# Optimization experiments

Measured on AMD Instinct MI355X. Metric: run time of the kernel, lower is better.

## Reference

```python
import jax, jax.numpy as jnp
import numpy as np


def _conv(x, w, stride):
    # Conv2d(k=3, stride, padding=1, bias=False), NCHW/OIHW
    return jax.lax.conv_general_dilated(
        x, w, (stride, stride), ((1, 1), (1, 1)),
        dimension_numbers=('NCHW', 'OIHW', 'NCHW'))


def _bn_silu(x, g, b, m, v):
    # BatchNorm2d (inference) + SiLU, fused elementwise
    scale = (g * jax.lax.rsqrt(v + 1e-5))[None, :, None, None]
    y = (x - m[None, :, None, None]) * scale + b[None, :, None, None]
    return y * jax.nn.sigmoid(y)


def _ss2d(x, in_w, dt_w, dt_b, B_w, C_w, A_log, D, out_w):
    # Low-rank 2D selective scan over flattened spatial tokens.
    Bn, C, H, W = x.shape
    L = H * W
    xt = x.reshape(Bn, C, L).transpose(0, 2, 1)            # [B,L,C]
    u = jnp.einsum('blc,rc->blr', xt, in_w)                # low-rank input [B,L,R]
    dt = jax.nn.softplus(jnp.einsum('blc,rc->blr', xt, dt_w) + dt_b)
    Bt = jnp.einsum('blc,nc->bln', xt, B_w)                # [B,L,N]
    Ct = jnp.einsum('blc,nc->bln', xt, C_w)                # [B,L,N]
    A = -jnp.exp(A_log)                                    # [R,N], stable (negative)

    def step(h, inp):
        u_t, dt_t, b_t, c_t = inp                          # [B,R],[B,R],[B,N],[B,N]
        dA = jnp.exp(dt_t[..., None] * A)                  # [B,R,N]
        h = dA * h + (dt_t[..., None] * b_t[:, None, :]) * u_t[..., None]
        y = jnp.einsum('brn,bn->br', h, c_t)               # [B,R]
        return h, (h, y)

    R, N = A_log.shape
    h0 = jnp.zeros((Bn, R, N), x.dtype)
    xs = (u.transpose(1, 0, 2), dt.transpose(1, 0, 2),
          Bt.transpose(1, 0, 2), Ct.transpose(1, 0, 2))
    _, (hs, ys) = jax.lax.scan(step, h0, xs)               # hs:[L,B,R,N] ys:[L,B,R]
    y = ys.transpose(1, 0, 2) + D * u                      # skip term D*u
    out = jnp.einsum('blr,cr->blc', y, out_w)              # project back to C
    x_out = (xt + out).transpose(0, 2, 1).reshape(Bn, C, H, W)
    state_seq = hs.transpose(1, 0, 2, 3)                   # [B,L,R,N]
    return x_out, state_seq


def setup_inputs() -> dict:
    key = jax.random.key(0)
    ks = jax.random.split(key, 24)
    f = jax.random.normal
    B, Cin, H, W = 8, 32, 112, 112
    E, R, N, NB = 64, 32, 64, 3
    inp = {}
    inp['x'] = f(ks[0], (B, Cin, H, W), jnp.float32)
    # stem
    inp['stem_w'] = f(ks[1], (E, Cin, 3, 3)) * 0.05
    inp['stem_g'] = 1.0 + 0.1 * f(ks[2], (E,))
    inp['stem_b'] = 0.1 * f(ks[3], (E,))
    inp['stem_m'] = 0.1 * f(ks[4], (E,))
    inp['stem_v'] = 1.0 + 0.1 * jax.random.uniform(ks[5], (E,))
    # SS2D blocks (stacked over num_blocks)
    inp['blk_in_w'] = f(ks[6], (NB, R, E)) * 0.1
    inp['blk_dt_w'] = f(ks[7], (NB, R, E)) * 0.05
    inp['blk_dt_b'] = f(ks[8], (NB, R)) * 0.1 - 2.0
    inp['blk_B_w'] = f(ks[9], (NB, N, E)) * 0.1
    inp['blk_C_w'] = f(ks[10], (NB, N, E)) * 0.1
    inp['blk_A_log'] = jnp.log(1.0 + jax.random.uniform(ks[11], (NB, R, N)) * 4.0)
    inp['blk_D'] = f(ks[12], (NB, R)) * 0.1
    inp['blk_out_w'] = f(ks[13], (NB, E, R)) * 0.1
    # down p4
    C4, C5 = 2 * E, 4 * E
    inp['p4_w'] = f(ks[14], (C4, E, 3, 3)) * 0.05
    inp['p4_g'] = 1.0 + 0.1 * f(ks[15], (C4,))
    inp['p4_b'] = 0.1 * f(ks[16], (C4,))
    inp['p4_m'] = 0.1 * f(ks[17], (C4,))
    inp['p4_v'] = 1.0 + 0.1 * jax.random.uniform(ks[18], (C4,))
    # down p5
    inp['p5_w'] = f(ks[19], (C5, C4, 3, 3)) * 0.05
    inp['p5_g'] = 1.0 + 0.1 * f(ks[20], (C5,))
    inp['p5_b'] = 0.1 * f(ks[21], (C5,))
    inp['p5_m'] = 0.1 * f(ks[22], (C5,))
    inp['p5_v'] = 1.0 + 0.1 * jax.random.uniform(ks[23], (C5,))
    return inp


def reference(x, stem_w, stem_g, stem_b, stem_m, stem_v,
              blk_in_w, blk_dt_w, blk_dt_b, blk_B_w, blk_C_w,
              blk_A_log, blk_D, blk_out_w,
              p4_w, p4_g, p4_b, p4_m, p4_v,
              p5_w, p5_g, p5_b, p5_m, p5_v):
    x = _bn_silu(_conv(x, stem_w, 2), stem_g, stem_b, stem_m, stem_v)
    states = []
    for i in range(blk_in_w.shape[0]):
        x, s = _ss2d(x, blk_in_w[i], blk_dt_w[i], blk_dt_b[i],
                     blk_B_w[i], blk_C_w[i], blk_A_log[i], blk_D[i], blk_out_w[i])
        states.append(s)
    p3 = x
    p4 = _bn_silu(_conv(p3, p4_w, 2), p4_g, p4_b, p4_m, p4_v)
    p5 = _bn_silu(_conv(p4, p5_w, 2), p5_g, p5_b, p5_m, p5_v)
    return (p3, p4, p5, jnp.stack(states))
```

## Files before the change

### kernel.cpp

```cpp
#include <hip/hip_runtime.h>
#include <cstdint>
#include <cstddef>

#define RFL(x) __builtin_amdgcn_readfirstlane(x)

constexpr int E  = 64;
constexpr int Rr = 32;
constexpr int Nn = 64;
constexpr int Lt = 3136;
constexpr int NC = 28;
constexpr int CL = 112;
constexpr int PD = 192;

__global__ __launch_bounds__(256) void k_wtrans(const float* __restrict__ in_w,
    const float* __restrict__ dt_w, const float* __restrict__ B_w,
    const float* __restrict__ C_w, float* __restrict__ wT) {
  int idx = blockIdx.x * 256 + threadIdx.x;
  if (idx >= 3 * 64 * PD) return;
  int o = idx % PD; int c = (idx / PD) & 63; int i = idx / (PD * 64);
  float v;
  if (o < 32)       v = in_w[(i * 32 + o) * 64 + c];
  else if (o < 64)  v = dt_w[(i * 32 + (o - 32)) * 64 + c];
  else if (o < 128) v = B_w[(i * 64 + (o - 64)) * 64 + c];
  else              v = C_w[(i * 64 + (o - 128)) * 64 + c];
  wT[idx] = v;
}

__global__ __launch_bounds__(256) void k_cwt2(const float* __restrict__ w,
    float* __restrict__ w3, int Cout, int Cin) {
  int idx = blockIdx.x * 256 + threadIdx.x;
  if (idx >= Cin * Cout * 9) return;
  int co = idx % Cout; int k = (idx / Cout) % 9; int ci = idx / (9 * Cout);
  w3[idx] = w[((size_t)co * Cin + ci) * 9 + k];
}

template<int CIN, int COUT, int HIN, int WIN>
__global__ __launch_bounds__(256) void k_conv(const float* __restrict__ x,
    const float* __restrict__ w3, const float* __restrict__ g, const float* __restrict__ bb,
    const float* __restrict__ m, const float* __restrict__ vv, float* __restrict__ out) {
  constexpr int HOUT = HIN / 2, WOUT = WIN / 2;
  constexpr int OWT = 7;
  constexpr int GWX = WOUT / OWT;
  constexpr int CIW = CIN / 4;
  __shared__ float xs[3][CIN][16];
  __shared__ float tbuf[4][64][8];

  int t = blockIdx.x;
  int b = t & 7; t >>= 3;
  int oh = t % HOUT; t /= HOUT;
  int gx = t % GWX; int cog = t / GWX;
  int lane = threadIdx.x & 63;
  int ws = RFL(threadIdx.x >> 6);
  int co = cog * 64 + lane;
  int iwb = gx * 14;
  int ih0 = oh * 2 - 1;

  for (int i = threadIdx.x; i < CIN * 3 * 16; i += 256) {
    int d = i & 15; int r3 = i >> 4;
    int kh = r3 / CIN; int ci = r3 & (CIN - 1);
    int iw = iwb + d - 1; int ih = ih0 + kh;
    float v = 0.f;
    if ((unsigned)iw < (unsigned)WIN && (unsigned)ih < (unsigned)HIN)
      v = x[(((size_t)(b * CIN + ci)) * HIN + ih) * WIN + iw];
    xs[kh][ci][d] = v;
  }
  __syncthreads();

  float acc[OWT];
#pragma unroll
  for (int o = 0; o < OWT; ++o) acc[o] = 0.f;

  int ci0 = ws * CIW;
#pragma unroll 2
  for (int cc = 0; cc < CIW; ++cc) {
    int ci = ci0 + cc;
    const float* wr = w3 + ((size_t)ci * 9) * COUT + co;
    float wk[9];
#pragma unroll
    for (int k = 0; k < 9; ++k) wk[k] = wr[(size_t)k * COUT];
#pragma unroll
    for (int kh = 0; kh < 3; ++kh) {
      const float4* tp4 = (const float4*)(&xs[kh][ci][0]);
      float4 q0 = tp4[0], q1 = tp4[1], q2 = tp4[2], q3 = tp4[3];
      float tp[16] = {q0.x, q0.y, q0.z, q0.w, q1.x, q1.y, q1.z, q1.w,
                      q2.x, q2.y, q2.z, q2.w, q3.x, q3.y, q3.z, q3.w};
#pragma unroll
      for (int o = 0; o < OWT; ++o) {
        acc[o] = fmaf(tp[2*o],     wk[kh*3+0], acc[o]);
        acc[o] = fmaf(tp[2*o + 1], wk[kh*3+1], acc[o]);
        acc[o] = fmaf(tp[2*o + 2], wk[kh*3+2], acc[o]);
      }
    }
  }
#pragma unroll
  for (int o = 0; o < OWT; ++o) tbuf[ws][lane][o] = acc[o];
  __syncthreads();

  for (int i = threadIdx.x; i < 64 * OWT; i += 256) {
    int cl = i / OWT, o = i - cl * OWT;
    float s = tbuf[0][cl][o] + tbuf[1][cl][o] + tbuf[2][cl][o] + tbuf[3][cl][o];
    int c2 = cog * 64 + cl;
    float scale = g[c2] * rsqrtf(vv[c2] + 1e-5f);
    float yv = (s - m[c2]) * scale + bb[c2];
    out[(((size_t)(b * COUT + c2)) * HOUT + oh) * WOUT + gx * OWT + o] =
        yv / (1.f + __expf(-yv));
  }
}

__global__ __launch_bounds__(256) void k_proj(const float* __restrict__ xin,
    const float* __restrict__ wT, const float* __restrict__ dt_b, float* __restrict__ P) {
  __shared__ float sm[64 * 196];
  int b = blockIdx.x & 7, tl = blockIdx.x >> 3;
  int l0 = tl * 64;
  int tid = threadIdx.x;
  for (int k = 0; k < 16; ++k) {
    int idx = k * 256 + tid; int c = idx >> 6, li = idx & 63;
    sm[c * 65 + li] = xin[(size_t)(b * 64 + c) * Lt + l0 + li];
  }
  __syncthreads();
  int tok = tid & 63;
  int og = RFL(tid >> 6);
  const float* wbase = wT + og * 48;
  float acc[48];
#pragma unroll
  for (int j = 0; j < 48; ++j) acc[j] = 0.f;
  for (int c = 0; c < 64; ++c) {
    float xv = sm[c * 65 + tok];
    const float4* w4 = (const float4*)(wbase + c * PD);
#pragma unroll
    for (int j = 0; j < 12; ++j) {
      float4 wv = __ldg(w4 + j);
      acc[4 * j + 0] = fmaf(xv, wv.x, acc[4 * j + 0]);
      acc[4 * j + 1] = fmaf(xv, wv.y, acc[4 * j + 1]);
      acc[4 * j + 2] = fmaf(xv, wv.z, acc[4 * j + 2]);
      acc[4 * j + 3] = fmaf(xv, wv.w, acc[4 * j + 3]);
    }
  }
  __syncthreads();
#pragma unroll
  for (int j = 0; j < 48; ++j) {
    int o = og * 48 + j;
    float v = acc[j];
    if (o >= 32 && o < 64) {
      v += dt_b[o - 32];
      v = fmaxf(v, 0.f) + log1pf(__expf(-fabsf(v)));
    }
    sm[tok * 196 + o] = v;
  }
  __syncthreads();
  float* dst = P + ((size_t)(b * Lt + l0)) * PD;
#pragma unroll
  for (int it = 0; it < 12; ++it) {
    int f = it * 1024 + tid * 4;
    int tk = f / 192;
    float4 v = *(const float4*)(&sm[tk * 196 + (f - tk * 192)]);
    *(float4*)(dst + f) = v;
  }
}

__global__ __launch_bounds__(256) void k_scan1(const float* __restrict__ P,
    const float* __restrict__ A_log, float* __restrict__ hfin, float* __restrict__ Pc) {
  __shared__ float xl[16][132];
  int bid = blockIdx.x;
  int b = bid & 7; int rest = bid >> 3;
  int c = rest % NC; int rg = rest / NC;
  int ws = RFL(threadIdx.x >> 6);
  int r = rg * 4 + ws;
  int n = threadIdx.x & 63;
  float a = -__expf(A_log[r * 64 + n]);
  const float* base = P + ((size_t)(b * Lt + c * CL)) * PD;
  int tl = threadIdx.x >> 4;
  int colb = (threadIdx.x & 15) * 8;
  float h = 0.f, sdt = 0.f;
  for (int s0 = 0; s0 < CL; s0 += 16) {
    __syncthreads();
    const float4* src = (const float4*)(base + (size_t)(s0 + tl) * PD + colb);
    float4 v0 = src[0], v1 = src[1];
    *(float4*)(&xl[tl][colb]) = v0;
    *(float4*)(&xl[tl][colb + 4]) = v1;
    __syncthreads();
#pragma unroll
    for (int tt = 0; tt < 16; ++tt) {
      float dt = xl[tt][32 + r];
      float u  = xl[tt][r];
      float bt = xl[tt][64 + n];
      h = fmaf(__expf(dt * a), h, (dt * u) * bt);
      sdt += dt;
    }
  }
  int o = ((b * 32 + r) * NC + c) * 64 + n;
  hfin[o] = h;
  Pc[o] = __expf(a * sdt);
}

__global__ __launch_bounds__(256) void k_scan2(const float* __restrict__ hfin,
    const float* __restrict__ Pc, float* __restrict__ Hs) {
  int wid = blockIdx.x * 4 + (threadIdx.x >> 6);
  int b = wid >> 5, r = wid & 31, n = threadIdx.x & 63;
  float H = 0.f;
  int base = ((b * 32 + r) * NC) * 64 + n;
#pragma unroll
  for (int c = 0; c < NC; ++c) {
    Hs[base + c * 64] = H;
    H = fmaf(Pc[base + c * 64], H, hfin[base + c * 64]);
  }
}

__global__ __launch_bounds__(256) void k_scan3(const float* __restrict__ P,
    const float* __restrict__ A_log, const float* __restrict__ Hs,
    const float* __restrict__ Dp, float* __restrict__ states, float* __restrict__ y) {
  __shared__ float xl[16][196];
  __shared__ __align__(16) float ylds[4][16][68];
  int bid = blockIdx.x;
  int b = bid & 7; int rest = bid >> 3;
  int c = rest % NC; int rg = rest / NC;
  int ws = RFL(threadIdx.x >> 6);
  int r = rg * 4 + ws;
  int n = threadIdx.x & 63;
  float a = -__expf(A_log[r * 64 + n]);
  float Dr = Dp[r];
  const float* base = P + ((size_t)(b * Lt + c * CL)) * PD;
  float h = Hs[((b * 32 + r) * NC + c) * 64 + n];
  float* st = states + ((size_t)(b * Lt + c * CL) * 32 + r) * 64 + n;
  float* yrow = y + (size_t)(b * 32 + r) * Lt + c * CL;
  int tl = threadIdx.x >> 4;
  int colb = (threadIdx.x & 15) * 12;
  for (int s0 = 0; s0 < CL; s0 += 16) {
    __syncthreads();
    const float4* src = (const float4*)(base + (size_t)(s0 + tl) * PD + colb);
    float4 v0 = src[0], v1 = src[1], v2 = src[2];
    *(float4*)(&xl[tl][colb])     = v0;
    *(float4*)(&xl[tl][colb + 4]) = v1;
    *(float4*)(&xl[tl][colb + 8]) = v2;
    __syncthreads();
#pragma unroll
    for (int tt = 0; tt < 16; ++tt) {
      float dt = xl[tt][32 + r];
      float u  = xl[tt][r];
      float bt = xl[tt][64 + n];
      float ct = xl[tt][128 + n];
      h = fmaf(__expf(dt * a), h, (dt * u) * bt);
      __builtin_nontemporal_store(h, st + (size_t)(s0 + tt) * 2048);
      ylds[ws][tt][n] = h * ct;
    }
    if (n < 16) {
      const float4* rp = (const float4*)(&ylds[ws][n][0]);
      float a0 = 0.f, a1 = 0.f, a2 = 0.f, a3 = 0.f;
#pragma unroll
      for (int k = 0; k < 16; ++k) {
        float4 pv = rp[k];
        a0 += pv.x; a1 += pv.y; a2 += pv.z; a3 += pv.w;
      }
      float sum = (a0 + a1) + (a2 + a3);
      float uu = xl[n][r];
      yrow[s0 + n] = sum + Dr * uu;
    }
  }
}

__global__ __launch_bounds__(256) void k_outproj(const float* __restrict__ xin,
    const float* __restrict__ y, const float* __restrict__ ow, float* __restrict__ xout) {
  __shared__ float ylds[32 * 64];
  int b = blockIdx.x & 7, tl = blockIdx.x >> 3;
  int l0 = tl * 64;
  int tid = threadIdx.x;
  for (int k = 0; k < 8; ++k) {
    int idx = k * 256 + tid; int r = idx >> 6, li = idx & 63;
    ylds[r * 64 + li] = y[(size_t)(b * 32 + r) * Lt + l0 + li];
  }
  __syncthreads();
  int li = tid & 63, cg = RFL(tid >> 6);
  for (int cc = 0; cc < 16; ++cc) {
    int ci = cg * 16 + cc;
    float acc = xin[(size_t)(b * 64 + ci) * Lt + l0 + li];
    const float4* w4 = (const float4*)(ow + ci * 32);
#pragma unroll
    for (int r4 = 0; r4 < 8; ++r4) {
      float4 wv = __ldg(w4 + r4);
      acc = fmaf(ylds[(r4 * 4 + 0) * 64 + li], wv.x, acc);
      acc = fmaf(ylds[(r4 * 4 + 1) * 64 + li], wv.y, acc);
      acc = fmaf(ylds[(r4 * 4 + 2) * 64 + li], wv.z, acc);
      acc = fmaf(ylds[(r4 * 4 + 3) * 64 + li], wv.w, acc);
    }
    xout[(size_t)(b * 64 + ci) * Lt + l0 + li] = acc;
  }
}

extern "C" void kernel_launch(void* const* d_in, const int* in_sizes, int n_in,
                              void* d_out, int out_size, void* d_ws, size_t ws_size,
                              hipStream_t stream) {
  const float* x      = (const float*)d_in[0];
  const float* stem_w = (const float*)d_in[1];
  const float* stem_g = (const float*)d_in[2];
  const float* stem_b = (const float*)d_in[3];
  const float* stem_m = (const float*)d_in[4];
  const float* stem_v = (const float*)d_in[5];
  const float* in_w   = (const float*)d_in[6];
  const float* dt_w   = (const float*)d_in[7];
  const float* dt_b   = (const float*)d_in[8];
  const float* B_w    = (const float*)d_in[9];
  const float* C_w    = (const float*)d_in[10];
  const float* A_log  = (const float*)d_in[11];
  const float* Dp     = (const float*)d_in[12];
  const float* out_w  = (const float*)d_in[13];
  const float* p4_w   = (const float*)d_in[14];
  const float* p4_g   = (const float*)d_in[15];
  const float* p4_b   = (const float*)d_in[16];
  const float* p4_m   = (const float*)d_in[17];
  const float* p4_v   = (const float*)d_in[18];
  const float* p5_w   = (const float*)d_in[19];
  const float* p5_g   = (const float*)d_in[20];
  const float* p5_b   = (const float*)d_in[21];
  const float* p5_m   = (const float*)d_in[22];
  const float* p5_v   = (const float*)d_in[23];

  float* out = (float*)d_out;
  float* wsf = (float*)d_ws;

  float* p3out = out;
  float* p4out = out + 1605632;
  float* p5out = out + 2408448;
  float* stout = out + 2809856;

  float* x0    = wsf;
  float* x1    = wsf + 1605632;
  float* Pb    = wsf + 3211264;
  float* yb    = wsf + 8028160;
  float* hfin  = wsf + 8830976;
  float* Pc    = wsf + 9289728;
  float* Hs    = wsf + 9748480;
  float* wT    = wsf + 10207232;
  float* w3s   = wsf + 10244096;
  float* w34   = wsf + 10262528;
  float* w35   = wsf + 10336256;

  k_wtrans<<<144, 256, 0, stream>>>(in_w, dt_w, B_w, C_w, wT);
  k_cwt2<<<72, 256, 0, stream>>>(stem_w, w3s, 64, 32);
  k_cwt2<<<288, 256, 0, stream>>>(p4_w, w34, 128, 64);
  k_cwt2<<<1152, 256, 0, stream>>>(p5_w, w35, 256, 128);

  k_conv<32, 64, 112, 112><<<3584, 256, 0, stream>>>(
      x, w3s, stem_g, stem_b, stem_m, stem_v, x0);

  const float* xi = x0;
  for (int i = 0; i < 3; ++i) {
    k_proj<<<392, 256, 0, stream>>>(xi, wT + i * 64 * PD, dt_b + i * 32, Pb);
    k_scan1<<<1792, 256, 0, stream>>>(Pb, A_log + i * 2048, hfin, Pc);
    k_scan2<<<64, 256, 0, stream>>>(hfin, Pc, Hs);
    k_scan3<<<1792, 256, 0, stream>>>(Pb, A_log + i * 2048, Hs, Dp + i * 32,
                                      stout + (size_t)i * 51380224, yb);
    float* dst = (i == 2) ? p3out : ((i == 0) ? x1 : x0);
    k_outproj<<<392, 256, 0, stream>>>(xi, yb, out_w + i * 2048, dst);
    xi = dst;
  }

  k_conv<64, 128, 56, 56><<<1792, 256, 0, stream>>>(
      p3out, w34, p4_g, p4_b, p4_m, p4_v, p4out);
  k_conv<128, 256, 28, 28><<<896, 256, 0, stream>>>(
      p4out, w35, p5_g, p5_b, p5_m, p5_v, p5out);
}
```

Before: 405.9 us.

## Interleave dt/u and B/C columns in projection buffer and parallelize y reduction

Result: slower. 436.9 us (+7.6%).

```diff
diff --git a/kernel.cpp b/kernel.cpp
--- a/kernel.cpp
+++ b/kernel.cpp
@@ -17,12 +17,15 @@
     const float* __restrict__ C_w, float* __restrict__ wT) {
   int idx = blockIdx.x * 256 + threadIdx.x;
   if (idx >= 3 * 64 * PD) return;
-  int o = idx % PD; int c = (idx / PD) & 63; int i = idx / (PD * 64);
+  int o = idx % PD; int cc = (idx / PD) & 63; int i = idx / (PD * 64);
   float v;
-  if (o < 32)       v = in_w[(i * 32 + o) * 64 + c];
-  else if (o < 64)  v = dt_w[(i * 32 + (o - 32)) * 64 + c];
-  else if (o < 128) v = B_w[(i * 64 + (o - 64)) * 64 + c];
-  else              v = C_w[(i * 64 + (o - 128)) * 64 + c];
+  if (o < 64) {
+    int r = o >> 1;
+    v = (o & 1) ? in_w[(i * 32 + r) * 64 + cc] : dt_w[(i * 32 + r) * 64 + cc];
+  } else {
+    int j = o - 64; int nn = j >> 1;
+    v = (j & 1) ? C_w[(i * 64 + nn) * 64 + cc] : B_w[(i * 64 + nn) * 64 + cc];
+  }
   wT[idx] = v;
 }
 
@@ -141,8 +144,8 @@
   for (int j = 0; j < 48; ++j) {
     int o = og * 48 + j;
     float v = acc[j];
-    if (o >= 32 && o < 64) {
-      v += dt_b[o - 32];
+    if (o < 64 && !(o & 1)) {
+      v += dt_b[o >> 1];
       v = fmaxf(v, 0.f) + log1pf(__expf(-fabsf(v)));
     }
     sm[tok * 196 + o] = v;
@@ -160,7 +163,7 @@
 
 __global__ __launch_bounds__(256) void k_scan1(const float* __restrict__ P,
     const float* __restrict__ A_log, float* __restrict__ hfin, float* __restrict__ Pc) {
-  __shared__ float xl[16][132];
+  __shared__ float xl[16][192];
   int bid = blockIdx.x;
   int b = bid & 7; int rest = bid >> 3;
   int c = rest % NC; int rg = rest / NC;
@@ -169,23 +172,20 @@
   int n = threadIdx.x & 63;
   float a = -__expf(A_log[r * 64 + n]);
   const float* base = P + ((size_t)(b * Lt + c * CL)) * PD;
-  int tl = threadIdx.x >> 4;
-  int colb = (threadIdx.x & 15) * 8;
   float h = 0.f, sdt = 0.f;
   for (int s0 = 0; s0 < CL; s0 += 16) {
     __syncthreads();
-    const float4* src = (const float4*)(base + (size_t)(s0 + tl) * PD + colb);
-    float4 v0 = src[0], v1 = src[1];
-    *(float4*)(&xl[tl][colb]) = v0;
-    *(float4*)(&xl[tl][colb + 4]) = v1;
+    for (int j = threadIdx.x; j < 768; j += 256) {
+      int tl = j / 48, c4 = (j - tl * 48) * 4;
+      *(float4*)(&xl[tl][c4]) = *(const float4*)(base + (size_t)(s0 + tl) * PD + c4);
+    }
     __syncthreads();
 #pragma unroll
     for (int tt = 0; tt < 16; ++tt) {
-      float dt = xl[tt][32 + r];
-      float u  = xl[tt][r];
-      float bt = xl[tt][64 + n];
-      h = fmaf(__expf(dt * a), h, (dt * u) * bt);
-      sdt += dt;
+      float2 du = *(const float2*)(&xl[tt][2 * r]);
+      float bt = xl[tt][64 + 2 * n];
+      h = fmaf(__expf(du.x * a), h, (du.x * du.y) * bt);
+      sdt += du.x;
     }
   }
   int o = ((b * 32 + r) * NC + c) * 64 + n;
@@ -209,7 +209,7 @@
 __global__ __launch_bounds__(256) void k_scan3(const float* __restrict__ P,
     const float* __restrict__ A_log, const float* __restrict__ Hs,
     const float* __restrict__ Dp, float* __restrict__ states, float* __restrict__ y) {
-  __shared__ float xl[16][196];
+  __shared__ float xl[16][200];
   __shared__ __align__(16) float ylds[4][16][68];
   int bid = blockIdx.x;
   int b = bid & 7; int rest = bid >> 3;
@@ -223,37 +223,33 @@
   float h = Hs[((b * 32 + r) * NC + c) * 64 + n];
   float* st = states + ((size_t)(b * Lt + c * CL) * 32 + r) * 64 + n;
   float* yrow = y + (size_t)(b * 32 + r) * Lt + c * CL;
-  int tl = threadIdx.x >> 4;
-  int colb = (threadIdx.x & 15) * 12;
+  int row = n >> 2, q = n & 3;
   for (int s0 = 0; s0 < CL; s0 += 16) {
     __syncthreads();
-    const float4* src = (const float4*)(base + (size_t)(s0 + tl) * PD + colb);
-    float4 v0 = src[0], v1 = src[1], v2 = src[2];
-    *(float4*)(&xl[tl][colb])     = v0;
-    *(float4*)(&xl[tl][colb + 4]) = v1;
-    *(float4*)(&xl[tl][colb + 8]) = v2;
+    for (int j = threadIdx.x; j < 768; j += 256) {
+      int tl = j / 48, c4 = (j - tl * 48) * 4;
+      *(float4*)(&xl[tl][c4]) = *(const float4*)(base + (size_t)(s0 + tl) * PD + c4);
+    }
     __syncthreads();
 #pragma unroll
     for (int tt = 0; tt < 16; ++tt) {
-      float dt = xl[tt][32 + r];
-      float u  = xl[tt][r];
-      float bt = xl[tt][64 + n];
-      float ct = xl[tt][128 + n];
-      h = fmaf(__expf(dt * a), h, (dt * u) * bt);
+      float2 du = *(const float2*)(&xl[tt][2 * r]);
+      float2 bc = *(const float2*)(&xl[tt][64 + 2 * n]);
+      h = fmaf(__expf(du.x * a), h, (du.x * du.y) * bc.x);
       __builtin_nontemporal_store(h, st + (size_t)(s0 + tt) * 2048);
-      ylds[ws][tt][n] = h * ct;
-    }
-    if (n < 16) {
-      const float4* rp = (const float4*)(&ylds[ws][n][0]);
-      float a0 = 0.f, a1 = 0.f, a2 = 0.f, a3 = 0.f;
-#pragma unroll
-      for (int k = 0; k < 16; ++k) {
-        float4 pv = rp[k];
-        a0 += pv.x; a1 += pv.y; a2 += pv.z; a3 += pv.w;
+      ylds[ws][tt][n] = h * bc.y;
+    }
+    {
+      const float4* rp = (const float4*)(&ylds[ws][row][q * 16]);
+      float4 p0 = rp[0], p1 = rp[1], p2 = rp[2], p3 = rp[3];
+      float p = ((p0.x + p0.y) + (p0.z + p0.w)) + ((p1.x + p1.y) + (p1.z + p1.w))
+              + ((p2.x + p2.y) + (p2.z + p2.w)) + ((p3.x + p3.y) + (p3.z + p3.w));
+      p += __shfl_xor(p, 1);
+      p += __shfl_xor(p, 2);
+      if (q == 0) {
+        float uu = xl[row][2 * r + 1];
+        yrow[s0 + row] = p + Dr * uu;
       }
-      float sum = (a0 + a1) + (a2 + a3);
-      float uu = xl[n][r];
-      yrow[s0 + n] = sum + Dr * uu;
     }
   }
 }
```

## Fuse chunk-local scan pass into projection kernel with 64-token chunks

Applied to the files above, without the earlier changes.

Result: slower. 432.2 us (+6.5%).

```diff
diff --git a/kernel.cpp b/kernel.cpp
--- a/kernel.cpp
+++ b/kernel.cpp
@@ -8,8 +8,8 @@
 constexpr int Rr = 32;
 constexpr int Nn = 64;
 constexpr int Lt = 3136;
-constexpr int NC = 28;
-constexpr int CL = 112;
+constexpr int NC = 49;
+constexpr int CL = 64;
 constexpr int PD = 192;
 
 __global__ __launch_bounds__(256) void k_wtrans(const float* __restrict__ in_w,
@@ -108,7 +108,9 @@
 }
 
 __global__ __launch_bounds__(256) void k_proj(const float* __restrict__ xin,
-    const float* __restrict__ wT, const float* __restrict__ dt_b, float* __restrict__ P) {
+    const float* __restrict__ wT, const float* __restrict__ dt_b,
+    const float* __restrict__ A_log, float* __restrict__ P,
+    float* __restrict__ hfin, float* __restrict__ Pc) {
   __shared__ float sm[64 * 196];
   int b = blockIdx.x & 7, tl = blockIdx.x >> 3;
   int l0 = tl * 64;
@@ -156,41 +158,31 @@
     float4 v = *(const float4*)(&sm[tk * 196 + (f - tk * 192)]);
     *(float4*)(dst + f) = v;
   }
-}
-
-__global__ __launch_bounds__(256) void k_scan1(const float* __restrict__ P,
-    const float* __restrict__ A_log, float* __restrict__ hfin, float* __restrict__ Pc) {
-  __shared__ float xl[16][132];
-  int bid = blockIdx.x;
-  int b = bid & 7; int rest = bid >> 3;
-  int c = rest % NC; int rg = rest / NC;
-  int ws = RFL(threadIdx.x >> 6);
-  int r = rg * 4 + ws;
-  int n = threadIdx.x & 63;
-  float a = -__expf(A_log[r * 64 + n]);
-  const float* base = P + ((size_t)(b * Lt + c * CL)) * PD;
-  int tl = threadIdx.x >> 4;
-  int colb = (threadIdx.x & 15) * 8;
-  float h = 0.f, sdt = 0.f;
-  for (int s0 = 0; s0 < CL; s0 += 16) {
-    __syncthreads();
-    const float4* src = (const float4*)(base + (size_t)(s0 + tl) * PD + colb);
-    float4 v0 = src[0], v1 = src[1];
-    *(float4*)(&xl[tl][colb]) = v0;
-    *(float4*)(&xl[tl][colb + 4]) = v1;
-    __syncthreads();
-#pragma unroll
-    for (int tt = 0; tt < 16; ++tt) {
-      float dt = xl[tt][32 + r];
-      float u  = xl[tt][r];
-      float bt = xl[tt][64 + n];
-      h = fmaf(__expf(dt * a), h, (dt * u) * bt);
-      sdt += dt;
-    }
-  }
-  int o = ((b * 32 + r) * NC + c) * 64 + n;
-  hfin[o] = h;
-  Pc[o] = __expf(a * sdt);
+  int n = tok;
+  int ws = og;
+  float a[8], h[8], sd[8];
+#pragma unroll
+  for (int k = 0; k < 8; ++k) {
+    a[k] = -__expf(A_log[(ws * 8 + k) * 64 + n]);
+    h[k] = 0.f; sd[k] = 0.f;
+  }
+  for (int t = 0; t < 64; ++t) {
+    const float* row = &sm[t * 196];
+    float bt = row[64 + n];
+#pragma unroll
+    for (int k = 0; k < 8; ++k) {
+      float dt = row[32 + ws * 8 + k];
+      float u  = row[ws * 8 + k];
+      h[k] = fmaf(__expf(dt * a[k]), h[k], (dt * u) * bt);
+      sd[k] += dt;
+    }
+  }
+#pragma unroll
+  for (int k = 0; k < 8; ++k) {
+    int o = ((b * 32 + ws * 8 + k) * NC + tl) * 64 + n;
+    hfin[o] = h[k];
+    Pc[o] = __expf(a[k] * sd[k]);
+  }
 }
 
 __global__ __launch_bounds__(256) void k_scan2(const float* __restrict__ hfin,
@@ -322,17 +314,18 @@
   float* p5out = out + 2408448;
   float* stout = out + 2809856;
 
+  float* x1 = stout + (size_t)2 * 51380224;
+
   float* x0    = wsf;
-  float* x1    = wsf + 1605632;
-  float* Pb    = wsf + 3211264;
-  float* yb    = wsf + 8028160;
-  float* hfin  = wsf + 8830976;
-  float* Pc    = wsf + 9289728;
-  float* Hs    = wsf + 9748480;
-  float* wT    = wsf + 10207232;
-  float* w3s   = wsf + 10244096;
-  float* w34   = wsf + 10262528;
-  float* w35   = wsf + 10336256;
+  float* Pb    = wsf + 1605632;
+  float* yb    = wsf + 6422528;
+  float* hfin  = wsf + 7225344;
+  float* Pc    = wsf + 8028160;
+  float* Hs    = wsf + 8830976;
+  float* wT    = wsf + 9633792;
+  float* w3s   = wsf + 9670656;
+  float* w34   = wsf + 9689088;
+  float* w35   = wsf + 9762816;
 
   k_wtrans<<<144, 256, 0, stream>>>(in_w, dt_w, B_w, C_w, wT);
   k_cwt2<<<72, 256, 0, stream>>>(stem_w, w3s, 64, 32);
@@ -344,10 +337,10 @@
 
   const float* xi = x0;
   for (int i = 0; i < 3; ++i) {
-    k_proj<<<392, 256, 0, stream>>>(xi, wT + i * 64 * PD, dt_b + i * 32, Pb);
-    k_scan1<<<1792, 256, 0, stream>>>(Pb, A_log + i * 2048, hfin, Pc);
+    k_proj<<<392, 256, 0, stream>>>(xi, wT + i * 64 * PD, dt_b + i * 32,
+                                    A_log + i * 2048, Pb, hfin, Pc);
     k_scan2<<<64, 256, 0, stream>>>(hfin, Pc, Hs);
-    k_scan3<<<1792, 256, 0, stream>>>(Pb, A_log + i * 2048, Hs, Dp + i * 32,
+    k_scan3<<<3136, 256, 0, stream>>>(Pb, A_log + i * 2048, Hs, Dp + i * 32,
                                       stout + (size_t)i * 51380224, yb);
     float* dst = (i == 2) ? p3out : ((i == 0) ? x1 : x0);
     k_outproj<<<392, 256, 0, stream>>>(xi, yb, out_w + i * 2048, dst);
```
